# Kernel optimization log

Measured on AMD Instinct MI355X. Metric: run time of the kernel, lower is better.

## Reference

```python
import jax, jax.numpy as jnp
import numpy as np

N_NODES = 50000
N_EDGES = 800000
NFEAT = 512
NHID = 64
NHEADS = 8
NCLASS = 40
ALPHA = 0.2  # LeakyReLU slope
EPS = 1e-16  # guards isolated-node division


def setup_inputs() -> dict:
    key = jax.random.key(0)
    k = jax.random.split(key, 6)
    x = jax.random.normal(k[0], (N_NODES, NFEAT), dtype=jnp.float32)
    W_heads = jax.random.normal(k[1], (NHEADS, NFEAT, NHID), dtype=jnp.float32) * 0.05
    a_heads = jax.random.normal(k[2], (NHEADS, 2 * NHID), dtype=jnp.float32) * 0.05
    W_out = jax.random.normal(k[3], (NHEADS * NHID, NCLASS), dtype=jnp.float32) * 0.05
    a_out = jax.random.normal(k[4], (2 * NCLASS,), dtype=jnp.float32) * 0.05
    edge_index = jax.random.randint(k[5], (2, N_EDGES), 0, N_NODES, dtype=jnp.int32)
    return {"x": x, "W_heads": W_heads, "a_heads": a_heads,
            "W_out": W_out, "a_out": a_out, "edge_index": edge_index}


def _gat_layer(x, W, a, row, col, concat):
    # pyGAT sparse layer: h = xW; e_ij = exp(-LeakyReLU(a^T [h_i || h_j]));
    # out_i = sum_j e_ij h_j / sum_j e_ij   (aggregate into row, gather from col)
    D = W.shape[1]
    h = x @ W                                            # [N, D]
    score = h[row] @ a[:D] + h[col] @ a[D:]              # [E]
    e = jnp.exp(-jax.nn.leaky_relu(score, ALPHA))        # [E]
    num = jax.ops.segment_sum(e[:, None] * h[col], row, num_segments=x.shape[0])  # [N, D]
    den = jax.ops.segment_sum(e, row, num_segments=x.shape[0])                    # [N]
    out = num / (den[:, None] + EPS)
    return jax.nn.elu(out) if concat else out


def reference(x, W_heads, a_heads, W_out, a_out, edge_index):
    # dropout layers are identity in eval mode (training=False)
    row, col = edge_index[0], edge_index[1]
    heads = jax.vmap(lambda W, a: _gat_layer(x, W, a, row, col, True))(W_heads, a_heads)
    # [H, N, D] -> [N, H*D] (concat along feature dim, head-major like torch.cat)
    hcat = jnp.transpose(heads, (1, 0, 2)).reshape(x.shape[0], -1)
    return _gat_layer(hcat, W_out, a_out, row, col, False)  # [N, NCLASS]
```

## Files before the change

kernel.cpp:

```cpp
#include <hip/hip_runtime.h>
#include <hip/hip_bf16.h>

#define N_NODES 50000
#define N_EDGES 800000
#define NFEAT   512
#define NHID    64
#define NHEADS  8
#define NCLASS  40
#define HD      (NHEADS*NHID)
#define ALPHA   0.2f
#define EPS_F   1e-16f
#define NCHUNK  ((N_NODES + 255)/256)

typedef __attribute__((ext_vector_type(8))) short short8;
typedef __attribute__((ext_vector_type(4))) float floatx4;

__device__ __forceinline__ float bf2f(unsigned short u) {
    union { unsigned int i; float f; } v; v.i = ((unsigned int)u) << 16; return v.f;
}
__device__ __forceinline__ unsigned short f2bf(float f) {
    union { __hip_bfloat16 h; unsigned short u; } cv;
    cv.h = __float2bfloat16(f);
    return cv.u;
}

__global__ void prep(const float* __restrict__ Wh, unsigned short* __restrict__ Wrb,
                     const float* __restrict__ Wo, unsigned short* __restrict__ Wob,
                     int* __restrict__ deg) {
    int idx = blockIdx.x*256 + threadIdx.x;
    if (idx >= 512*512) return;
    if (idx < N_NODES) deg[idx] = 0;
    {
        int n = idx >> 9, k = idx & 511;
        int hd = n >> 6, d = n & 63;
        Wrb[idx] = f2bf(Wh[(size_t)hd*NFEAT*NHID + (size_t)k*NHID + d]);
    }
    if (idx < 64*512) {
        int n = idx >> 9, k = idx & 511;
        float v = (n < NCLASS) ? Wo[(size_t)k*NCLASS + n] : 0.f;
        Wob[idx] = f2bf(v);
    }
}

__global__ __launch_bounds__(256) void mfma_gemm1(const float* __restrict__ A,
                                                  const unsigned short* __restrict__ Bbf,
                                                  unsigned short* __restrict__ H1p, int M) {
    int id = blockIdx.x;
    int rb = (id >> 5)*8 + (id & 7);
    int cb = (id >> 3) & 3;
    int row0 = rb * 128, col0 = cb * 128;
    if (row0 >= M) return;

    __shared__ short Asl[128*40];
    __shared__ short Bsl[128*40];
    int tid  = threadIdx.x;
    int wid  = tid >> 6, lane = tid & 63;
    int lrow = lane & 15, quad = lane >> 4;
    int wm = wid & 1, wn = wid >> 1;

    int sr[2], sk[2];
#pragma unroll
    for (int it = 0; it < 2; ++it) {
        int q = tid + it*256;
        sr[it] = q >> 2; sk[it] = (q & 3) * 8;
    }
    int arow[2];
#pragma unroll
    for (int it = 0; it < 2; ++it) {
        int ar = row0 + sr[it];
        arow[it] = ar < M ? ar : M - 1;
    }

    floatx4 acc[4][4];
#pragma unroll
    for (int mm = 0; mm < 4; mm++)
#pragma unroll
        for (int nn = 0; nn < 4; nn++) acc[mm][nn] = (floatx4){0.f,0.f,0.f,0.f};

    float4 fa[2][2];
    short8 fb[2];
#pragma unroll
    for (int it = 0; it < 2; ++it) {
        const float* src = A + (size_t)arow[it]*512 + sk[it];
        fa[it][0] = *(const float4*)src;
        fa[it][1] = *(const float4*)(src + 4);
        fb[it] = *(const short8*)(Bbf + (size_t)(col0 + sr[it])*512 + sk[it]);
    }

    for (int k0 = 0; k0 < 512; k0 += 32) {
#pragma unroll
        for (int it = 0; it < 2; ++it) {
            short8 h;
            h[0] = (short)f2bf(fa[it][0].x); h[1] = (short)f2bf(fa[it][0].y);
            h[2] = (short)f2bf(fa[it][0].z); h[3] = (short)f2bf(fa[it][0].w);
            h[4] = (short)f2bf(fa[it][1].x); h[5] = (short)f2bf(fa[it][1].y);
            h[6] = (short)f2bf(fa[it][1].z); h[7] = (short)f2bf(fa[it][1].w);
            *(short8*)(&Asl[sr[it]*40 + sk[it]]) = h;
            *(short8*)(&Bsl[sr[it]*40 + sk[it]]) = fb[it];
        }
        __syncthreads();
        if (k0 + 32 < 512) {
            int kn = k0 + 32;
#pragma unroll
            for (int it = 0; it < 2; ++it) {
                const float* src = A + (size_t)arow[it]*512 + kn + sk[it];
                fa[it][0] = *(const float4*)src;
                fa[it][1] = *(const float4*)(src + 4);
                fb[it] = *(const short8*)(Bbf + (size_t)(col0 + sr[it])*512 + kn + sk[it]);
            }
        }
        short8 af[4], bfr[4];
#pragma unroll
        for (int mm = 0; mm < 4; ++mm)
            af[mm] = *(const short8*)(&Asl[(wm*64 + mm*16 + lrow)*40 + quad*8]);
#pragma unroll
        for (int nn = 0; nn < 4; ++nn)
            bfr[nn] = *(const short8*)(&Bsl[(wn*64 + nn*16 + lrow)*40 + quad*8]);
#pragma unroll
        for (int mm = 0; mm < 4; ++mm)
#pragma unroll
            for (int nn = 0; nn < 4; ++nn)
                acc[mm][nn] = __builtin_amdgcn_mfma_f32_16x16x32_bf16(
                    af[mm], bfr[nn], acc[mm][nn], 0, 0, 0);
        __syncthreads();
    }

#pragma unroll
    for (int mm = 0; mm < 4; ++mm) {
        int rbase = row0 + wm*64 + mm*16 + quad*4;
#pragma unroll
        for (int nn = 0; nn < 4; ++nn) {
            int c = col0 + wn*64 + nn*16 + lrow;
            int off = (c & 63)*8 + (c >> 6);
#pragma unroll
            for (int r = 0; r < 4; ++r) {
                int grow = rbase + r;
                if (grow < M)
                    H1p[(size_t)grow*512 + off] = f2bf(acc[mm][nn][r]);
            }
        }
    }
}

__global__ __launch_bounds__(256) void mfma_gemm2(const unsigned short* __restrict__ Abf,
                                                  const unsigned short* __restrict__ Bbf,
                                                  float* __restrict__ H2p, int M) {
    __shared__ short Asl[256*40];
    __shared__ short Bsl[64*40];
    int tid  = threadIdx.x;
    int wid  = tid >> 6, lane = tid & 63;
    int lrow = lane & 15, quad = lane >> 4;
    int row0 = blockIdx.x * 256;

    floatx4 acc[4][4];
#pragma unroll
    for (int mm = 0; mm < 4; mm++)
#pragma unroll
        for (int nn = 0; nn < 4; nn++) acc[mm][nn] = (floatx4){0.f,0.f,0.f,0.f};

    for (int k0 = 0; k0 < 512; k0 += 32) {
#pragma unroll
        for (int it = 0; it < 4; ++it) {
            int q  = tid + it*256;
            int r  = q >> 2, kk = (q & 3) * 8;
            int ar = row0 + r; ar = ar < M ? ar : M - 1;
            *(short8*)(&Asl[r*40 + kk]) =
                *(const short8*)(Abf + (size_t)ar*512 + k0 + kk);
        }
        {
            int r = tid >> 2, kk = (tid & 3) * 8;
            *(short8*)(&Bsl[r*40 + kk]) =
                *(const short8*)(Bbf + (size_t)r*512 + k0 + kk);
        }
        __syncthreads();
        short8 af[4], bfr[4];
#pragma unroll
        for (int mm = 0; mm < 4; ++mm)
            af[mm] = *(const short8*)(&Asl[(wid*64 + mm*16 + lrow)*40 + quad*8]);
#pragma unroll
        for (int nn = 0; nn < 4; ++nn)
            bfr[nn] = *(const short8*)(&Bsl[(nn*16 + lrow)*40 + quad*8]);
#pragma unroll
        for (int mm = 0; mm < 4; ++mm)
#pragma unroll
            for (int nn = 0; nn < 4; ++nn)
                acc[mm][nn] = __builtin_amdgcn_mfma_f32_16x16x32_bf16(
                    af[mm], bfr[nn], acc[mm][nn], 0, 0, 0);
        __syncthreads();
    }

#pragma unroll
    for (int mm = 0; mm < 4; ++mm) {
        int rbase = row0 + wid*64 + mm*16 + quad*4;
#pragma unroll
        for (int nn = 0; nn < 4; ++nn) {
            int c = nn*16 + lrow;
#pragma unroll
            for (int r = 0; r < 4; ++r) {
                int grow = rbase + r;
                if (grow < M)
                    H2p[(size_t)grow*64 + c] = acc[mm][nn][r];
            }
        }
    }
}

__global__ __launch_bounds__(256) void dots1(const unsigned short* __restrict__ H1p,
                                             const float* __restrict__ a_heads,
                                             float* __restrict__ srcdot,
                                             float* __restrict__ dstdot) {
    int wave = (blockIdx.x*256 + threadIdx.x) >> 6;
    int lane = threadIdx.x & 63;
    if (wave >= N_NODES) return;
    short8 hv = *(const short8*)(H1p + (size_t)wave*512 + lane*8);
    float s0[8], s1[8];
#pragma unroll
    for (int j = 0; j < 8; j++) {
        float h = bf2f((unsigned short)hv[j]);
        s0[j] = h * a_heads[j*128 + lane];
        s1[j] = h * a_heads[j*128 + 64 + lane];
    }
#pragma unroll
    for (int off = 32; off > 0; off >>= 1) {
#pragma unroll
        for (int j = 0; j < 8; j++) {
            s0[j] += __shfl_down(s0[j], off, 64);
            s1[j] += __shfl_down(s1[j], off, 64);
        }
    }
    if (lane == 0) {
#pragma unroll
        for (int j = 0; j < 8; j++) {
            srcdot[wave*8 + j] = s0[j];
            dstdot[wave*8 + j] = s1[j];
        }
    }
}

__global__ void histk(const int* __restrict__ row, int* __restrict__ deg) {
    int e = blockIdx.x*256 + threadIdx.x;
    if (e < N_EDGES) atomicAdd(&deg[row[e]], 1);
}
__global__ void scanA(const int* __restrict__ deg, int* __restrict__ row_ptr,
                      int* __restrict__ chunk_tot) {
    __shared__ int s[256];
    int t = threadIdx.x;
    int idx = blockIdx.x*256 + t;
    int v = (idx < N_NODES) ? deg[idx] : 0;
    s[t] = v;
    __syncthreads();
#pragma unroll
    for (int off = 1; off < 256; off <<= 1) {
        int x = (t >= off) ? s[t-off] : 0;
        __syncthreads();
        s[t] += x;
        __syncthreads();
    }
    if (idx < N_NODES) row_ptr[idx] = s[t] - v;
    if (t == 255) chunk_tot[blockIdx.x] = s[t];
}
__global__ void scanB(const int* __restrict__ chunk_tot, int* __restrict__ chunk_off,
                      int* __restrict__ row_ptr) {
    __shared__ int s[256];
    int t = threadIdx.x;
    int v = (t < NCHUNK) ? chunk_tot[t] : 0;
    s[t] = v;
    __syncthreads();
#pragma unroll
    for (int off = 1; off < 256; off <<= 1) {
        int x = (t >= off) ? s[t-off] : 0;
        __syncthreads();
        s[t] += x;
        __syncthreads();
    }
    if (t < NCHUNK) chunk_off[t] = s[t] - v;
    if (t == 255) row_ptr[N_NODES] = s[t];
}
__global__ void scanC(const int* __restrict__ chunk_off, int* __restrict__ row_ptr,
                      int* __restrict__ cursor) {
    int idx = blockIdx.x*256 + threadIdx.x;
    if (idx < N_NODES) {
        int rp = row_ptr[idx] + chunk_off[idx >> 8];
        row_ptr[idx] = rp;
        cursor[idx] = rp;
    }
}

__global__ void fillk_w1(const int* __restrict__ row, const int* __restrict__ col,
                         const float* __restrict__ srcdot, const float* __restrict__ dstdot,
                         int* __restrict__ cursor, int* __restrict__ csr_col,
                         float* __restrict__ Wcsr) {
    int e = blockIdx.x*256 + threadIdx.x;
    if (e >= N_EDGES) return;
    int r = row[e], c = col[e];
    int pos = atomicAdd(&cursor[r], 1);
    csr_col[pos] = c;
    float4 sa = *(const float4*)(srcdot + (size_t)r*8);
    float4 sb = *(const float4*)(srcdot + (size_t)r*8 + 4);
    float4 da = *(const float4*)(dstdot + (size_t)c*8);
    float4 db = *(const float4*)(dstdot + (size_t)c*8 + 4);
    float s[8] = {sa.x+da.x, sa.y+da.y, sa.z+da.z, sa.w+da.w,
                  sb.x+db.x, sb.y+db.y, sb.z+db.z, sb.w+db.w};
    float o[8];
#pragma unroll
    for (int j = 0; j < 8; j++) {
        float lr = s[j] > 0.f ? s[j] : ALPHA*s[j];
        o[j] = __expf(-lr);
    }
    *(float4*)(Wcsr + (size_t)pos*8)     = make_float4(o[0], o[1], o[2], o[3]);
    *(float4*)(Wcsr + (size_t)pos*8 + 4) = make_float4(o[4], o[5], o[6], o[7]);
}

__global__ __launch_bounds__(256) void agg1(const unsigned short* __restrict__ H1p,
                                            const float* __restrict__ Wcsr,
                                            const int* __restrict__ row_ptr,
                                            const int* __restrict__ csr_col,
                                            unsigned short* __restrict__ hcatb) {
    int wave = (blockIdx.x*256 + threadIdx.x) >> 6;
    int lane = threadIdx.x & 63;
    if (wave >= N_NODES) return;
    int start = row_ptr[wave], end = row_ptr[wave+1];
    float acc[8], den[8];
#pragma unroll
    for (int j = 0; j < 8; j++) { acc[j] = 0.f; den[j] = 0.f; }

    int k = start;
    for (; k + 4 <= end; k += 4) {
        int c0 = csr_col[k],   c1 = csr_col[k+1];
        int c2 = csr_col[k+2], c3 = csr_col[k+3];
        short8 hv0 = *(const short8*)(H1p + (size_t)c0*512 + lane*8);
        short8 hv1 = *(const short8*)(H1p + (size_t)c1*512 + lane*8);
        short8 hv2 = *(const short8*)(H1p + (size_t)c2*512 + lane*8);
        short8 hv3 = *(const short8*)(H1p + (size_t)c3*512 + lane*8);
        float4 wv[8];
#pragma unroll
        for (int q = 0; q < 8; q++)
            wv[q] = *(const float4*)(Wcsr + (size_t)k*8 + q*4);
        const float* w0 = (const float*)&wv[0];
        const float* w1 = (const float*)&wv[2];
        const float* w2 = (const float*)&wv[4];
        const float* w3 = (const float*)&wv[6];
#pragma unroll
        for (int j = 0; j < 8; j++) {
            den[j] += (w0[j] + w1[j]) + (w2[j] + w3[j]);
            acc[j] = fmaf(w0[j], bf2f((unsigned short)hv0[j]), acc[j]);
            acc[j] = fmaf(w1[j], bf2f((unsigned short)hv1[j]), acc[j]);
            acc[j] = fmaf(w2[j], bf2f((unsigned short)hv2[j]), acc[j]);
            acc[j] = fmaf(w3[j], bf2f((unsigned short)hv3[j]), acc[j]);
        }
    }
    for (; k < end; ++k) {
        int c = csr_col[k];
        float4 wa = *(const float4*)(Wcsr + (size_t)k*8);
        float4 wb = *(const float4*)(Wcsr + (size_t)k*8 + 4);
        short8 hv = *(const short8*)(H1p + (size_t)c*512 + lane*8);
        float w[8] = {wa.x, wa.y, wa.z, wa.w, wb.x, wb.y, wb.z, wb.w};
#pragma unroll
        for (int j = 0; j < 8; j++) {
            den[j] += w[j];
            acc[j] = fmaf(w[j], bf2f((unsigned short)hv[j]), acc[j]);
        }
    }
#pragma unroll
    for (int j = 0; j < 8; j++) {
        float o = acc[j] / (den[j] + EPS_F);
        o = o > 0.f ? o : (__expf(o) - 1.f);
        hcatb[(size_t)wave*HD + j*64 + lane] = f2bf(o);
    }
}

__global__ void dots2(const float* __restrict__ H2p, const float* __restrict__ a_out,
                      float* __restrict__ src2, float* __restrict__ dst2) {
    int i = blockIdx.x*256 + threadIdx.x;
    if (i >= N_NODES) return;
    float s0 = 0.f, s1 = 0.f;
#pragma unroll
    for (int c = 0; c < NCLASS; c++) {
        float h = H2p[(size_t)i*64 + c];
        s0 = fmaf(h, a_out[c], s0);
        s1 = fmaf(h, a_out[NCLASS + c], s1);
    }
    src2[i] = s0; dst2[i] = s1;
}

__global__ __launch_bounds__(256) void agg2(const float* __restrict__ H2p,
                                            const float* __restrict__ src2,
                                            const float* __restrict__ dst2,
                                            const int* __restrict__ row_ptr,
                                            const int* __restrict__ csr_col,
                                            float* __restrict__ out) {
    int wave = (blockIdx.x*256 + threadIdx.x) >> 6;
    int lane = threadIdx.x & 63;
    if (wave >= N_NODES) return;
    int start = row_ptr[wave], end = row_ptr[wave+1];
    float s2i = src2[wave];
    int l = lane < NCLASS ? lane : 0;
    float acc = 0.f, den = 0.f;
    int k = start;
    for (; k + 4 <= end; k += 4) {
        int c0 = csr_col[k],   c1 = csr_col[k+1];
        int c2 = csr_col[k+2], c3 = csr_col[k+3];
        float t0 = s2i + dst2[c0], t1 = s2i + dst2[c1];
        float t2 = s2i + dst2[c2], t3 = s2i + dst2[c3];
        float h0 = H2p[(size_t)c0*64 + l];
        float h1 = H2p[(size_t)c1*64 + l];
        float h2 = H2p[(size_t)c2*64 + l];
        float h3 = H2p[(size_t)c3*64 + l];
        t0 = t0 > 0.f ? t0 : ALPHA*t0;  float w0 = __expf(-t0);
        t1 = t1 > 0.f ? t1 : ALPHA*t1;  float w1 = __expf(-t1);
        t2 = t2 > 0.f ? t2 : ALPHA*t2;  float w2 = __expf(-t2);
        t3 = t3 > 0.f ? t3 : ALPHA*t3;  float w3 = __expf(-t3);
        den += (w0 + w1) + (w2 + w3);
        acc = fmaf(w0, h0, acc);
        acc = fmaf(w1, h1, acc);
        acc = fmaf(w2, h2, acc);
        acc = fmaf(w3, h3, acc);
    }
    for (; k < end; ++k) {
        int c = csr_col[k];
        float t = s2i + dst2[c];
        t = t > 0.f ? t : ALPHA*t;
        float w = __expf(-t);
        den += w;
        acc = fmaf(w, H2p[(size_t)c*64 + l], acc);
    }
    if (lane < NCLASS)
        out[(size_t)wave*NCLASS + lane] = acc / (den + EPS_F);
}

extern "C" void kernel_launch(void* const* d_in, const int* in_sizes, int n_in,
                              void* d_out, int out_size, void* d_ws, size_t ws_size,
                              hipStream_t stream) {
    const float* x       = (const float*)d_in[0];
    const float* W_heads = (const float*)d_in[1];
    const float* a_heads = (const float*)d_in[2];
    const float* W_out   = (const float*)d_in[3];
    const float* a_out   = (const float*)d_in[4];
    const int*   ei      = (const int*)d_in[5];
    const int*   row     = ei;
    const int*   col     = ei + N_EDGES;
    float* out = (float*)d_out;

    char* ws = (char*)d_ws;
    size_t off = 0;
    auto alloc = [&](size_t bytes) {
        char* p = ws + off;
        off = (off + bytes + 255) & ~(size_t)255;
        return p;
    };
    unsigned short* Wrb   = (unsigned short*)alloc((size_t)512*512*2);
    unsigned short* Wob   = (unsigned short*)alloc((size_t)64*512*2);
    unsigned short* H1p   = (unsigned short*)alloc((size_t)N_NODES*HD*2);
    unsigned short* hcatb = (unsigned short*)alloc((size_t)N_NODES*HD*2);
    float* srcdot  = (float*)alloc((size_t)N_NODES*NHEADS*4);
    float* dstdot  = (float*)alloc((size_t)N_NODES*NHEADS*4);
    float* Wcsr    = (float*)alloc((size_t)N_EDGES*NHEADS*4);
    int*   deg     = (int*)alloc((size_t)N_NODES*4);
    int*   row_ptr = (int*)alloc((size_t)(N_NODES+1)*4);
    int*   cursor  = (int*)alloc((size_t)N_NODES*4);
    int*   ctot    = (int*)alloc(256*4);
    int*   coff    = (int*)alloc(256*4);
    int*   csr_col = (int*)alloc((size_t)N_EDGES*4);
    float* H2p     = (float*)alloc((size_t)N_NODES*64*4);
    float* src2    = (float*)alloc((size_t)N_NODES*4);
    float* dst2    = (float*)alloc((size_t)N_NODES*4);
    (void)ws_size;

    const int EB = (N_EDGES + 255)/256;
    const int WB = (N_NODES*64 + 255)/256;
    const int NB = (N_NODES + 255)/256;

    prep<<<(512*512 + 255)/256, 256, 0, stream>>>(W_heads, Wrb, W_out, Wob, deg);
    {
        int rtiles = (N_NODES + 127)/128;
        int nblk = ((rtiles + 7)/8) * 32;
        mfma_gemm1<<<nblk, 256, 0, stream>>>(x, Wrb, H1p, N_NODES);
    }
    dots1<<<WB, 256, 0, stream>>>(H1p, a_heads, srcdot, dstdot);

    histk<<<EB, 256, 0, stream>>>(row, deg);
    scanA<<<NCHUNK, 256, 0, stream>>>(deg, row_ptr, ctot);
    scanB<<<1, 256, 0, stream>>>(ctot, coff, row_ptr);
    scanC<<<NCHUNK, 256, 0, stream>>>(coff, row_ptr, cursor);
    fillk_w1<<<EB, 256, 0, stream>>>(row, col, srcdot, dstdot, cursor,
                                     csr_col, Wcsr);

    agg1<<<WB, 256, 0, stream>>>(H1p, Wcsr, row_ptr, csr_col, hcatb);

    mfma_gemm2<<<(N_NODES + 255)/256, 256, 0, stream>>>(hcatb, Wob, H2p, N_NODES);
    dots2<<<NB, 256, 0, stream>>>(H2p, a_out, src2, dst2);
    agg2<<<WB, 256, 0, stream>>>(H2p, src2, dst2, row_ptr, csr_col, out);
}
```

Baseline: 551.6 us.

## Compute edge attention weights inside agg1, preload columns via readlane, pipeline gathers

Stops materializing per-edge attention weights (Wcsr) in the CSR fill kernel. agg1 now recomputes them on the fly from srcdot and gathered dstdot. Both aggregation kernels load up to 64 neighbor indices once per wave into a register, broadcast them with readlane, and double-buffer the gathers so the next batch loads while the current one is consumed. dots2 moves to one wave per node with a shuffle reduction. The aim is to cut the 25.6MB write and read of Wcsr and the serialized index loads, at the cost of redundant exp work and higher register pressure.

```diff
diff --git a/kernel.cpp b/kernel.cpp
--- a/kernel.cpp
+++ b/kernel.cpp
@@ -286,33 +286,18 @@
     }
 }
 
-__global__ void fillk_w1(const int* __restrict__ row, const int* __restrict__ col,
-                         const float* __restrict__ srcdot, const float* __restrict__ dstdot,
-                         int* __restrict__ cursor, int* __restrict__ csr_col,
-                         float* __restrict__ Wcsr) {
+__global__ void fillk(const int* __restrict__ row, const int* __restrict__ col,
+                      int* __restrict__ cursor, int* __restrict__ csr_col) {
     int e = blockIdx.x*256 + threadIdx.x;
     if (e >= N_EDGES) return;
     int r = row[e], c = col[e];
     int pos = atomicAdd(&cursor[r], 1);
     csr_col[pos] = c;
-    float4 sa = *(const float4*)(srcdot + (size_t)r*8);
-    float4 sb = *(const float4*)(srcdot + (size_t)r*8 + 4);
-    float4 da = *(const float4*)(dstdot + (size_t)c*8);
-    float4 db = *(const float4*)(dstdot + (size_t)c*8 + 4);
-    float s[8] = {sa.x+da.x, sa.y+da.y, sa.z+da.z, sa.w+da.w,
-                  sb.x+db.x, sb.y+db.y, sb.z+db.z, sb.w+db.w};
-    float o[8];
-#pragma unroll
-    for (int j = 0; j < 8; j++) {
-        float lr = s[j] > 0.f ? s[j] : ALPHA*s[j];
-        o[j] = __expf(-lr);
-    }
-    *(float4*)(Wcsr + (size_t)pos*8)     = make_float4(o[0], o[1], o[2], o[3]);
-    *(float4*)(Wcsr + (size_t)pos*8 + 4) = make_float4(o[4], o[5], o[6], o[7]);
 }
 
 __global__ __launch_bounds__(256) void agg1(const unsigned short* __restrict__ H1p,
-                                            const float* __restrict__ Wcsr,
+                                            const float* __restrict__ srcdot,
+                                            const float* __restrict__ dstdot,
                                             const int* __restrict__ row_ptr,
                                             const int* __restrict__ csr_col,
                                             unsigned short* __restrict__ hcatb) {
@@ -320,67 +305,123 @@
     int lane = threadIdx.x & 63;
     if (wave >= N_NODES) return;
     int start = row_ptr[wave], end = row_ptr[wave+1];
-    float acc[8], den[8];
-#pragma unroll
-    for (int j = 0; j < 8; j++) { acc[j] = 0.f; den[j] = 0.f; }
-
+    int deg = end - start;
+
+    float4 sa = *(const float4*)(srcdot + (size_t)wave*8);
+    float4 sb = *(const float4*)(srcdot + (size_t)wave*8 + 4);
+    float sd0 = sa.x, sd1 = sa.y, sd2 = sa.z, sd3 = sa.w;
+    float sd4 = sb.x, sd5 = sb.y, sd6 = sb.z, sd7 = sb.w;
+
+    float acc0=0.f,acc1=0.f,acc2=0.f,acc3=0.f,acc4=0.f,acc5=0.f,acc6=0.f,acc7=0.f;
+    float den0=0.f,den1=0.f,den2=0.f,den3=0.f,den4=0.f,den5=0.f,den6=0.f,den7=0.f;
+
+    int colreg = 0;
+    if (deg > 0) colreg = csr_col[start + (lane < deg ? lane : deg - 1)];
+
+#define CONS1(H, D0, D1) do { \
+    float t0_=sd0+(D0).x, t1_=sd1+(D0).y, t2_=sd2+(D0).z, t3_=sd3+(D0).w; \
+    float t4_=sd4+(D1).x, t5_=sd5+(D1).y, t6_=sd6+(D1).z, t7_=sd7+(D1).w; \
+    t0_ = t0_>0.f?t0_:ALPHA*t0_; t1_ = t1_>0.f?t1_:ALPHA*t1_; \
+    t2_ = t2_>0.f?t2_:ALPHA*t2_; t3_ = t3_>0.f?t3_:ALPHA*t3_; \
+    t4_ = t4_>0.f?t4_:ALPHA*t4_; t5_ = t5_>0.f?t5_:ALPHA*t5_; \
+    t6_ = t6_>0.f?t6_:ALPHA*t6_; t7_ = t7_>0.f?t7_:ALPHA*t7_; \
+    float w0_=__expf(-t0_), w1_=__expf(-t1_), w2_=__expf(-t2_), w3_=__expf(-t3_); \
+    float w4_=__expf(-t4_), w5_=__expf(-t5_), w6_=__expf(-t6_), w7_=__expf(-t7_); \
+    den0+=w0_; acc0=fmaf(w0_, bf2f((unsigned short)(H)[0]), acc0); \
+    den1+=w1_; acc1=fmaf(w1_, bf2f((unsigned short)(H)[1]), acc1); \
+    den2+=w2_; acc2=fmaf(w2_, bf2f((unsigned short)(H)[2]), acc2); \
+    den3+=w3_; acc3=fmaf(w3_, bf2f((unsigned short)(H)[3]), acc3); \
+    den4+=w4_; acc4=fmaf(w4_, bf2f((unsigned short)(H)[4]), acc4); \
+    den5+=w5_; acc5=fmaf(w5_, bf2f((unsigned short)(H)[5]), acc5); \
+    den6+=w6_; acc6=fmaf(w6_, bf2f((unsigned short)(H)[6]), acc6); \
+    den7+=w7_; acc7=fmaf(w7_, bf2f((unsigned short)(H)[7]), acc7); \
+} while(0)
+
+#define GATH3(HS0,HS1,HS2,P0,P1,P2,P3,P4,P5,BASE) do { \
+    int cg0_ = __builtin_amdgcn_readlane(colreg, (BASE)); \
+    int cg1_ = __builtin_amdgcn_readlane(colreg, (BASE)+1); \
+    int cg2_ = __builtin_amdgcn_readlane(colreg, (BASE)+2); \
+    HS0 = *(const short8*)(H1p + (size_t)cg0_*512 + lane*8); \
+    P0  = *(const float4*)(dstdot + (size_t)cg0_*8); \
+    P1  = *(const float4*)(dstdot + (size_t)cg0_*8 + 4); \
+    HS1 = *(const short8*)(H1p + (size_t)cg1_*512 + lane*8); \
+    P2  = *(const float4*)(dstdot + (size_t)cg1_*8); \
+    P3  = *(const float4*)(dstdot + (size_t)cg1_*8 + 4); \
+    HS2 = *(const short8*)(H1p + (size_t)cg2_*512 + lane*8); \
+    P4  = *(const float4*)(dstdot + (size_t)cg2_*8); \
+    P5  = *(const float4*)(dstdot + (size_t)cg2_*8 + 4); \
+} while(0)
+
+#define CONS3(HS0,HS1,HS2,P0,P1,P2,P3,P4,P5) do { \
+    CONS1(HS0,P0,P1); CONS1(HS1,P2,P3); CONS1(HS2,P4,P5); } while(0)
+
+    int lim = deg < 64 ? deg : 64;
+    int nb = lim / 3;
     int k = start;
-    for (; k + 4 <= end; k += 4) {
-        int c0 = csr_col[k],   c1 = csr_col[k+1];
-        int c2 = csr_col[k+2], c3 = csr_col[k+3];
-        short8 hv0 = *(const short8*)(H1p + (size_t)c0*512 + lane*8);
-        short8 hv1 = *(const short8*)(H1p + (size_t)c1*512 + lane*8);
-        short8 hv2 = *(const short8*)(H1p + (size_t)c2*512 + lane*8);
-        short8 hv3 = *(const short8*)(H1p + (size_t)c3*512 + lane*8);
-        float4 wv[8];
-#pragma unroll
-        for (int q = 0; q < 8; q++)
-            wv[q] = *(const float4*)(Wcsr + (size_t)k*8 + q*4);
-        const float* w0 = (const float*)&wv[0];
-        const float* w1 = (const float*)&wv[2];
-        const float* w2 = (const float*)&wv[4];
-        const float* w3 = (const float*)&wv[6];
+    short8 ha0, ha1, ha2, hb0, hb1, hb2;
+    float4 pa0, pa1, pa2, pa3, pa4, pa5;
+    float4 pb0, pb1, pb2, pb3, pb4, pb5;
+    if (nb > 0) {
+        GATH3(ha0,ha1,ha2, pa0,pa1,pa2,pa3,pa4,pa5, 0);
+        int b = 1;
+        for (; b + 1 < nb; b += 2) {
+            GATH3(hb0,hb1,hb2, pb0,pb1,pb2,pb3,pb4,pb5, b*3);
+            CONS3(ha0,ha1,ha2, pa0,pa1,pa2,pa3,pa4,pa5);
+            GATH3(ha0,ha1,ha2, pa0,pa1,pa2,pa3,pa4,pa5, (b+1)*3);
+            CONS3(hb0,hb1,hb2, pb0,pb1,pb2,pb3,pb4,pb5);
+        }
+        if (b < nb) {
+            GATH3(hb0,hb1,hb2, pb0,pb1,pb2,pb3,pb4,pb5, b*3);
+            CONS3(ha0,ha1,ha2, pa0,pa1,pa2,pa3,pa4,pa5);
+            CONS3(hb0,hb1,hb2, pb0,pb1,pb2,pb3,pb4,pb5);
+        } else {
+            CONS3(ha0,ha1,ha2, pa0,pa1,pa2,pa3,pa4,pa5);
+        }
+        k = start + nb*3;
+    }
+    for (; k < end; ++k) {
+        int c_ = (k - start < 64) ? __builtin_amdgcn_readlane(colreg, k - start)
+                                  : csr_col[k];
+        short8 hv = *(const short8*)(H1p + (size_t)c_*512 + lane*8);
+        float4 d0 = *(const float4*)(dstdot + (size_t)c_*8);
+        float4 d1 = *(const float4*)(dstdot + (size_t)c_*8 + 4);
+        CONS1(hv, d0, d1);
+    }
+#undef GATH3
+#undef CONS3
+
+    {
+        float o, dsum;
+        float accv[8] = {acc0,acc1,acc2,acc3,acc4,acc5,acc6,acc7};
+        float denv[8] = {den0,den1,den2,den3,den4,den5,den6,den7};
 #pragma unroll
         for (int j = 0; j < 8; j++) {
-            den[j] += (w0[j] + w1[j]) + (w2[j] + w3[j]);
-            acc[j] = fmaf(w0[j], bf2f((unsigned short)hv0[j]), acc[j]);
-            acc[j] = fmaf(w1[j], bf2f((unsigned short)hv1[j]), acc[j]);
-            acc[j] = fmaf(w2[j], bf2f((unsigned short)hv2[j]), acc[j]);
-            acc[j] = fmaf(w3[j], bf2f((unsigned short)hv3[j]), acc[j]);
-        }
-    }
-    for (; k < end; ++k) {
-        int c = csr_col[k];
-        float4 wa = *(const float4*)(Wcsr + (size_t)k*8);
-        float4 wb = *(const float4*)(Wcsr + (size_t)k*8 + 4);
-        short8 hv = *(const short8*)(H1p + (size_t)c*512 + lane*8);
-        float w[8] = {wa.x, wa.y, wa.z, wa.w, wb.x, wb.y, wb.z, wb.w};
-#pragma unroll
-        for (int j = 0; j < 8; j++) {
-            den[j] += w[j];
-            acc[j] = fmaf(w[j], bf2f((unsigned short)hv[j]), acc[j]);
-        }
-    }
-#pragma unroll
-    for (int j = 0; j < 8; j++) {
-        float o = acc[j] / (den[j] + EPS_F);
-        o = o > 0.f ? o : (__expf(o) - 1.f);
-        hcatb[(size_t)wave*HD + j*64 + lane] = f2bf(o);
-    }
-}
-
-__global__ void dots2(const float* __restrict__ H2p, const float* __restrict__ a_out,
-                      float* __restrict__ src2, float* __restrict__ dst2) {
-    int i = blockIdx.x*256 + threadIdx.x;
-    if (i >= N_NODES) return;
-    float s0 = 0.f, s1 = 0.f;
-#pragma unroll
-    for (int c = 0; c < NCLASS; c++) {
-        float h = H2p[(size_t)i*64 + c];
-        s0 = fmaf(h, a_out[c], s0);
-        s1 = fmaf(h, a_out[NCLASS + c], s1);
-    }
-    src2[i] = s0; dst2[i] = s1;
+            dsum = denv[j];
+            o = accv[j] / (dsum + EPS_F);
+            o = o > 0.f ? o : (__expf(o) - 1.f);
+            hcatb[(size_t)wave*HD + j*64 + lane] = f2bf(o);
+        }
+    }
+#undef CONS1
+}
+
+__global__ __launch_bounds__(256) void dots2(const float* __restrict__ H2p,
+                                             const float* __restrict__ a_out,
+                                             float* __restrict__ src2,
+                                             float* __restrict__ dst2) {
+    int wave = (blockIdx.x*256 + threadIdx.x) >> 6;
+    int lane = threadIdx.x & 63;
+    if (wave >= N_NODES) return;
+    float h  = H2p[(size_t)wave*64 + lane];
+    float a0 = lane < NCLASS ? a_out[lane] : 0.f;
+    float a1 = lane < NCLASS ? a_out[NCLASS + lane] : 0.f;
+    float s0 = h * a0, s1 = h * a1;
+#pragma unroll
+    for (int off = 32; off > 0; off >>= 1) {
+        s0 += __shfl_down(s0, off, 64);
+        s1 += __shfl_down(s1, off, 64);
+    }
+    if (lane == 0) { src2[wave] = s0; dst2[wave] = s1; }
 }
 
 __global__ __launch_bounds__(256) void agg2(const float* __restrict__ H2p,
@@ -393,37 +434,71 @@
     int lane = threadIdx.x & 63;
     if (wave >= N_NODES) return;
     int start = row_ptr[wave], end = row_ptr[wave+1];
+    int deg = end - start;
     float s2i = src2[wave];
     int l = lane < NCLASS ? lane : 0;
     float acc = 0.f, den = 0.f;
+
+    int colreg = 0;
+    if (deg > 0) colreg = csr_col[start + (lane < deg ? lane : deg - 1)];
+
+#define AG2_G1(T, H, IDX) do { \
+    int cg_ = __builtin_amdgcn_readlane(colreg, (IDX)); \
+    T = dst2[cg_]; \
+    H = H2p[(size_t)cg_*64 + l]; \
+} while(0)
+#define AG2_C1(T, H) do { \
+    float t_ = s2i + (T); \
+    t_ = t_ > 0.f ? t_ : ALPHA*t_; \
+    float w_ = __expf(-t_); \
+    den += w_; acc = fmaf(w_, (H), acc); \
+} while(0)
+#define AG2_G8(T0,T1,T2,T3,T4,T5,T6,T7,H0,H1,H2,H3,H4,H5,H6,H7,BASE) do { \
+    AG2_G1(T0,H0,(BASE));   AG2_G1(T1,H1,(BASE)+1); \
+    AG2_G1(T2,H2,(BASE)+2); AG2_G1(T3,H3,(BASE)+3); \
+    AG2_G1(T4,H4,(BASE)+4); AG2_G1(T5,H5,(BASE)+5); \
+    AG2_G1(T6,H6,(BASE)+6); AG2_G1(T7,H7,(BASE)+7); \
+} while(0)
+#define AG2_C8(T0,T1,T2,T3,T4,T5,T6,T7,H0,H1,H2,H3,H4,H5,H6,H7) do { \
+    AG2_C1(T0,H0); AG2_C1(T1,H1); AG2_C1(T2,H2); AG2_C1(T3,H3); \
+    AG2_C1(T4,H4); AG2_C1(T5,H5); AG2_C1(T6,H6); AG2_C1(T7,H7); \
+} while(0)
+
+    int lim = deg < 64 ? deg : 64;
+    int nb = lim >> 3;
     int k = start;
-    for (; k + 4 <= end; k += 4) {
-        int c0 = csr_col[k],   c1 = csr_col[k+1];
-        int c2 = csr_col[k+2], c3 = csr_col[k+3];
-        float t0 = s2i + dst2[c0], t1 = s2i + dst2[c1];
-        float t2 = s2i + dst2[c2], t3 = s2i + dst2[c3];
-        float h0 = H2p[(size_t)c0*64 + l];
-        float h1 = H2p[(size_t)c1*64 + l];
-        float h2 = H2p[(size_t)c2*64 + l];
-        float h3 = H2p[(size_t)c3*64 + l];
-        t0 = t0 > 0.f ? t0 : ALPHA*t0;  float w0 = __expf(-t0);
-        t1 = t1 > 0.f ? t1 : ALPHA*t1;  float w1 = __expf(-t1);
-        t2 = t2 > 0.f ? t2 : ALPHA*t2;  float w2 = __expf(-t2);
-        t3 = t3 > 0.f ? t3 : ALPHA*t3;  float w3 = __expf(-t3);
-        den += (w0 + w1) + (w2 + w3);
-        acc = fmaf(w0, h0, acc);
-        acc = fmaf(w1, h1, acc);
-        acc = fmaf(w2, h2, acc);
-        acc = fmaf(w3, h3, acc);
+    float ta0,ta1,ta2,ta3,ta4,ta5,ta6,ta7, ga0,ga1,ga2,ga3,ga4,ga5,ga6,ga7;
+    float tb0,tb1,tb2,tb3,tb4,tb5,tb6,tb7, gb0,gb1,gb2,gb3,gb4,gb5,gb6,gb7;
+    if (nb > 0) {
+        AG2_G8(ta0,ta1,ta2,ta3,ta4,ta5,ta6,ta7, ga0,ga1,ga2,ga3,ga4,ga5,ga6,ga7, 0);
+        int b = 1;
+        for (; b + 1 < nb; b += 2) {
+            AG2_G8(tb0,tb1,tb2,tb3,tb4,tb5,tb6,tb7, gb0,gb1,gb2,gb3,gb4,gb5,gb6,gb7, b*8);
+            AG2_C8(ta0,ta1,ta2,ta3,ta4,ta5,ta6,ta7, ga0,ga1,ga2,ga3,ga4,ga5,ga6,ga7);
+            AG2_G8(ta0,ta1,ta2,ta3,ta4,ta5,ta6,ta7, ga0,ga1,ga2,ga3,ga4,ga5,ga6,ga7, (b+1)*8);
+            AG2_C8(tb0,tb1,tb2,tb3,tb4,tb5,tb6,tb7, gb0,gb1,gb2,gb3,gb4,gb5,gb6,gb7);
+        }
+        if (b < nb) {
+            AG2_G8(tb0,tb1,tb2,tb3,tb4,tb5,tb6,tb7, gb0,gb1,gb2,gb3,gb4,gb5,gb6,gb7, b*8);
+            AG2_C8(ta0,ta1,ta2,ta3,ta4,ta5,ta6,ta7, ga0,ga1,ga2,ga3,ga4,ga5,ga6,ga7);
+            AG2_C8(tb0,tb1,tb2,tb3,tb4,tb5,tb6,tb7, gb0,gb1,gb2,gb3,gb4,gb5,gb6,gb7);
+        } else {
+            AG2_C8(ta0,ta1,ta2,ta3,ta4,ta5,ta6,ta7, ga0,ga1,ga2,ga3,ga4,ga5,ga6,ga7);
+        }
+        k = start + nb*8;
     }
     for (; k < end; ++k) {
-        int c = csr_col[k];
-        float t = s2i + dst2[c];
-        t = t > 0.f ? t : ALPHA*t;
-        float w = __expf(-t);
-        den += w;
-        acc = fmaf(w, H2p[(size_t)c*64 + l], acc);
-    }
+        int c_ = (k - start < 64) ? __builtin_amdgcn_readlane(colreg, k - start)
+                                  : csr_col[k];
+        float t = dst2[c_];
+        float h = H2p[(size_t)c_*64 + l];
+        AG2_C1(t, h);
+    }
+#undef AG2_G1
+#undef AG2_C1
+#undef AG2_G8
+#undef AG2_C8
+
     if (lane < NCLASS)
         out[(size_t)wave*NCLASS + lane] = acc / (den + EPS_F);
 }
@@ -454,7 +529,6 @@
     unsigned short* hcatb = (unsigned short*)alloc((size_t)N_NODES*HD*2);
     float* srcdot  = (float*)alloc((size_t)N_NODES*NHEADS*4);
     float* dstdot  = (float*)alloc((size_t)N_NODES*NHEADS*4);
-    float* Wcsr    = (float*)alloc((size_t)N_EDGES*NHEADS*4);
     int*   deg     = (int*)alloc((size_t)N_NODES*4);
     int*   row_ptr = (int*)alloc((size_t)(N_NODES+1)*4);
     int*   cursor  = (int*)alloc((size_t)N_NODES*4);
@@ -468,7 +542,6 @@
 
     const int EB = (N_EDGES + 255)/256;
     const int WB = (N_NODES*64 + 255)/256;
-    const int NB = (N_NODES + 255)/256;
 
     prep<<<(512*512 + 255)/256, 256, 0, stream>>>(W_heads, Wrb, W_out, Wob, deg);
     {
@@ -482,12 +555,11 @@
     scanA<<<NCHUNK, 256, 0, stream>>>(deg, row_ptr, ctot);
     scanB<<<1, 256, 0, stream>>>(ctot, coff, row_ptr);
     scanC<<<NCHUNK, 256, 0, stream>>>(coff, row_ptr, cursor);
-    fillk_w1<<<EB, 256, 0, stream>>>(row, col, srcdot, dstdot, cursor,
-                                     csr_col, Wcsr);
-
-    agg1<<<WB, 256, 0, stream>>>(H1p, Wcsr, row_ptr, csr_col, hcatb);
+    fillk<<<EB, 256, 0, stream>>>(row, col, cursor, csr_col);
+
+    agg1<<<WB, 256, 0, stream>>>(H1p, srcdot, dstdot, row_ptr, csr_col, hcatb);
 
     mfma_gemm2<<<(N_NODES + 255)/256, 256, 0, stream>>>(hcatb, Wob, H2p, N_NODES);
-    dots2<<<NB, 256, 0, stream>>>(H2p, a_out, src2, dst2);
+    dots2<<<WB, 256, 0, stream>>>(H2p, a_out, src2, dst2);
     agg2<<<WB, 256, 0, stream>>>(H2p, src2, dst2, row_ptr, csr_col, out);
 }
```

New measurement: 565.8 us. 2.6% more time.

## Fuse attention dot products into GEMM epilogues and pipeline agg2 gathers

Applied to the files above, without the earlier changes.

Computes the per-head source and destination attention dot products directly from the MFMA accumulators in both GEMM epilogues, using 16-lane xor shuffles, and removes the separate dots1 and dots2 kernels. This avoids re-reading H1p and H2p and saves two launches. agg2 now loads up to 64 column indices into a register once, broadcasts them with readlane, and software-pipelines gathers in batches of 8 with double buffering to raise memory-level parallelism. The cost is higher register pressure, and the dot products now use fp32 accumulators instead of bf16-rounded values, which slightly changes numerics.

```diff
diff --git a/kernel.cpp b/kernel.cpp
--- a/kernel.cpp
+++ b/kernel.cpp
@@ -44,7 +44,10 @@
 
 __global__ __launch_bounds__(256) void mfma_gemm1(const float* __restrict__ A,
                                                   const unsigned short* __restrict__ Bbf,
-                                                  unsigned short* __restrict__ H1p, int M) {
+                                                  const float* __restrict__ a_heads,
+                                                  unsigned short* __restrict__ H1p,
+                                                  float* __restrict__ srcdot,
+                                                  float* __restrict__ dstdot, int M) {
     int id = blockIdx.x;
     int rb = (id >> 5)*8 + (id & 7);
     int cb = (id >> 3) & 3;
@@ -125,6 +128,39 @@
         __syncthreads();
     }
 
+    {
+        int head = (col0 >> 6) + wn;
+        float a0v[4], a1v[4];
+#pragma unroll
+        for (int nn = 0; nn < 4; ++nn) {
+            a0v[nn] = a_heads[head*128 + nn*16 + lrow];
+            a1v[nn] = a_heads[head*128 + 64 + nn*16 + lrow];
+        }
+#pragma unroll
+        for (int mm = 0; mm < 4; ++mm) {
+#pragma unroll
+            for (int r = 0; r < 4; ++r) {
+                float s0 = 0.f, s1 = 0.f;
+#pragma unroll
+                for (int nn = 0; nn < 4; ++nn) {
+                    float v = acc[mm][nn][r];
+                    s0 = fmaf(v, a0v[nn], s0);
+                    s1 = fmaf(v, a1v[nn], s1);
+                }
+#pragma unroll
+                for (int off = 1; off < 16; off <<= 1) {
+                    s0 += __shfl_xor(s0, off, 64);
+                    s1 += __shfl_xor(s1, off, 64);
+                }
+                int grow = row0 + wm*64 + mm*16 + quad*4 + r;
+                if (lrow == 0 && grow < M) {
+                    srcdot[(size_t)grow*8 + head] = s0;
+                    dstdot[(size_t)grow*8 + head] = s1;
+                }
+            }
+        }
+    }
+
 #pragma unroll
     for (int mm = 0; mm < 4; ++mm) {
         int rbase = row0 + wm*64 + mm*16 + quad*4;
@@ -144,7 +180,10 @@
 
 __global__ __launch_bounds__(256) void mfma_gemm2(const unsigned short* __restrict__ Abf,
                                                   const unsigned short* __restrict__ Bbf,
-                                                  float* __restrict__ H2p, int M) {
+                                                  const float* __restrict__ a_out,
+                                                  float* __restrict__ H2p,
+                                                  float* __restrict__ src2,
+                                                  float* __restrict__ dst2, int M) {
     __shared__ short Asl[256*40];
     __shared__ short Bsl[64*40];
     int tid  = threadIdx.x;
@@ -189,6 +228,39 @@
         __syncthreads();
     }
 
+    {
+        float a0v[4], a1v[4];
+#pragma unroll
+        for (int nn = 0; nn < 4; ++nn) {
+            int c = nn*16 + lrow;
+            a0v[nn] = c < NCLASS ? a_out[c] : 0.f;
+            a1v[nn] = c < NCLASS ? a_out[NCLASS + c] : 0.f;
+        }
+#pragma unroll
+        for (int mm = 0; mm < 4; ++mm) {
+#pragma unroll
+            for (int r = 0; r < 4; ++r) {
+                float s0 = 0.f, s1 = 0.f;
+#pragma unroll
+                for (int nn = 0; nn < 4; ++nn) {
+                    float v = acc[mm][nn][r];
+                    s0 = fmaf(v, a0v[nn], s0);
+                    s1 = fmaf(v, a1v[nn], s1);
+                }
+#pragma unroll
+                for (int off = 1; off < 16; off <<= 1) {
+                    s0 += __shfl_xor(s0, off, 64);
+                    s1 += __shfl_xor(s1, off, 64);
+                }
+                int grow = row0 + wid*64 + mm*16 + quad*4 + r;
+                if (lrow == 0 && grow < M) {
+                    src2[grow] = s0;
+                    dst2[grow] = s1;
+                }
+            }
+        }
+    }
+
 #pragma unroll
     for (int mm = 0; mm < 4; ++mm) {
         int rbase = row0 + wid*64 + mm*16 + quad*4;
@@ -201,38 +273,6 @@
                 if (grow < M)
                     H2p[(size_t)grow*64 + c] = acc[mm][nn][r];
             }
-        }
-    }
-}
-
-__global__ __launch_bounds__(256) void dots1(const unsigned short* __restrict__ H1p,
-                                             const float* __restrict__ a_heads,
-                                             float* __restrict__ srcdot,
-                                             float* __restrict__ dstdot) {
-    int wave = (blockIdx.x*256 + threadIdx.x) >> 6;
-    int lane = threadIdx.x & 63;
-    if (wave >= N_NODES) return;
-    short8 hv = *(const short8*)(H1p + (size_t)wave*512 + lane*8);
-    float s0[8], s1[8];
-#pragma unroll
-    for (int j = 0; j < 8; j++) {
-        float h = bf2f((unsigned short)hv[j]);
-        s0[j] = h * a_heads[j*128 + lane];
-        s1[j] = h * a_heads[j*128 + 64 + lane];
-    }
-#pragma unroll
-    for (int off = 32; off > 0; off >>= 1) {
-#pragma unroll
-        for (int j = 0; j < 8; j++) {
-            s0[j] += __shfl_down(s0[j], off, 64);
-            s1[j] += __shfl_down(s1[j], off, 64);
-        }
-    }
-    if (lane == 0) {
-#pragma unroll
-        for (int j = 0; j < 8; j++) {
-            srcdot[wave*8 + j] = s0[j];
-            dstdot[wave*8 + j] = s1[j];
         }
     }
 }
@@ -369,20 +409,6 @@
     }
 }
 
-__global__ void dots2(const float* __restrict__ H2p, const float* __restrict__ a_out,
-                      float* __restrict__ src2, float* __restrict__ dst2) {
-    int i = blockIdx.x*256 + threadIdx.x;
-    if (i >= N_NODES) return;
-    float s0 = 0.f, s1 = 0.f;
-#pragma unroll
-    for (int c = 0; c < NCLASS; c++) {
-        float h = H2p[(size_t)i*64 + c];
-        s0 = fmaf(h, a_out[c], s0);
-        s1 = fmaf(h, a_out[NCLASS + c], s1);
-    }
-    src2[i] = s0; dst2[i] = s1;
-}
-
 __global__ __launch_bounds__(256) void agg2(const float* __restrict__ H2p,
                                             const float* __restrict__ src2,
                                             const float* __restrict__ dst2,
@@ -393,37 +419,71 @@
     int lane = threadIdx.x & 63;
     if (wave >= N_NODES) return;
     int start = row_ptr[wave], end = row_ptr[wave+1];
+    int deg = end - start;
     float s2i = src2[wave];
     int l = lane < NCLASS ? lane : 0;
     float acc = 0.f, den = 0.f;
+
+    int colreg = 0;
+    if (deg > 0) colreg = csr_col[start + (lane < deg ? lane : deg - 1)];
+
+#define AG2_G1(T, H, IDX) do { \
+    int cg_ = __builtin_amdgcn_readlane(colreg, (IDX)); \
+    T = dst2[cg_]; \
+    H = H2p[(size_t)cg_*64 + l]; \
+} while(0)
+#define AG2_C1(T, H) do { \
+    float t_ = s2i + (T); \
+    t_ = t_ > 0.f ? t_ : ALPHA*t_; \
+    float w_ = __expf(-t_); \
+    den += w_; acc = fmaf(w_, (H), acc); \
+} while(0)
+#define AG2_G8(T0,T1,T2,T3,T4,T5,T6,T7,H0,H1,H2,H3,H4,H5,H6,H7,BASE) do { \
+    AG2_G1(T0,H0,(BASE));   AG2_G1(T1,H1,(BASE)+1); \
+    AG2_G1(T2,H2,(BASE)+2); AG2_G1(T3,H3,(BASE)+3); \
+    AG2_G1(T4,H4,(BASE)+4); AG2_G1(T5,H5,(BASE)+5); \
+    AG2_G1(T6,H6,(BASE)+6); AG2_G1(T7,H7,(BASE)+7); \
+} while(0)
+#define AG2_C8(T0,T1,T2,T3,T4,T5,T6,T7,H0,H1,H2,H3,H4,H5,H6,H7) do { \
+    AG2_C1(T0,H0); AG2_C1(T1,H1); AG2_C1(T2,H2); AG2_C1(T3,H3); \
+    AG2_C1(T4,H4); AG2_C1(T5,H5); AG2_C1(T6,H6); AG2_C1(T7,H7); \
+} while(0)
+
+    int lim = deg < 64 ? deg : 64;
+    int nb = lim >> 3;
     int k = start;
-    for (; k + 4 <= end; k += 4) {
-        int c0 = csr_col[k],   c1 = csr_col[k+1];
-        int c2 = csr_col[k+2], c3 = csr_col[k+3];
-        float t0 = s2i + dst2[c0], t1 = s2i + dst2[c1];
-        float t2 = s2i + dst2[c2], t3 = s2i + dst2[c3];
-        float h0 = H2p[(size_t)c0*64 + l];
-        float h1 = H2p[(size_t)c1*64 + l];
-        float h2 = H2p[(size_t)c2*64 + l];
-        float h3 = H2p[(size_t)c3*64 + l];
-        t0 = t0 > 0.f ? t0 : ALPHA*t0;  float w0 = __expf(-t0);
-        t1 = t1 > 0.f ? t1 : ALPHA*t1;  float w1 = __expf(-t1);
-        t2 = t2 > 0.f ? t2 : ALPHA*t2;  float w2 = __expf(-t2);
-        t3 = t3 > 0.f ? t3 : ALPHA*t3;  float w3 = __expf(-t3);
-        den += (w0 + w1) + (w2 + w3);
-        acc = fmaf(w0, h0, acc);
-        acc = fmaf(w1, h1, acc);
-        acc = fmaf(w2, h2, acc);
-        acc = fmaf(w3, h3, acc);
+    float ta0,ta1,ta2,ta3,ta4,ta5,ta6,ta7, ga0,ga1,ga2,ga3,ga4,ga5,ga6,ga7;
+    float tb0,tb1,tb2,tb3,tb4,tb5,tb6,tb7, gb0,gb1,gb2,gb3,gb4,gb5,gb6,gb7;
+    if (nb > 0) {
+        AG2_G8(ta0,ta1,ta2,ta3,ta4,ta5,ta6,ta7, ga0,ga1,ga2,ga3,ga4,ga5,ga6,ga7, 0);
+        int b = 1;
+        for (; b + 1 < nb; b += 2) {
+            AG2_G8(tb0,tb1,tb2,tb3,tb4,tb5,tb6,tb7, gb0,gb1,gb2,gb3,gb4,gb5,gb6,gb7, b*8);
+            AG2_C8(ta0,ta1,ta2,ta3,ta4,ta5,ta6,ta7, ga0,ga1,ga2,ga3,ga4,ga5,ga6,ga7);
+            AG2_G8(ta0,ta1,ta2,ta3,ta4,ta5,ta6,ta7, ga0,ga1,ga2,ga3,ga4,ga5,ga6,ga7, (b+1)*8);
+            AG2_C8(tb0,tb1,tb2,tb3,tb4,tb5,tb6,tb7, gb0,gb1,gb2,gb3,gb4,gb5,gb6,gb7);
+        }
+        if (b < nb) {
+            AG2_G8(tb0,tb1,tb2,tb3,tb4,tb5,tb6,tb7, gb0,gb1,gb2,gb3,gb4,gb5,gb6,gb7, b*8);
+            AG2_C8(ta0,ta1,ta2,ta3,ta4,ta5,ta6,ta7, ga0,ga1,ga2,ga3,ga4,ga5,ga6,ga7);
+            AG2_C8(tb0,tb1,tb2,tb3,tb4,tb5,tb6,tb7, gb0,gb1,gb2,gb3,gb4,gb5,gb6,gb7);
+        } else {
+            AG2_C8(ta0,ta1,ta2,ta3,ta4,ta5,ta6,ta7, ga0,ga1,ga2,ga3,ga4,ga5,ga6,ga7);
+        }
+        k = start + nb*8;
     }
     for (; k < end; ++k) {
-        int c = csr_col[k];
-        float t = s2i + dst2[c];
-        t = t > 0.f ? t : ALPHA*t;
-        float w = __expf(-t);
-        den += w;
-        acc = fmaf(w, H2p[(size_t)c*64 + l], acc);
-    }
+        int c_ = (k - start < 64) ? __builtin_amdgcn_readlane(colreg, k - start)
+                                  : csr_col[k];
+        float t = dst2[c_];
+        float h = H2p[(size_t)c_*64 + l];
+        AG2_C1(t, h);
+    }
+#undef AG2_G1
+#undef AG2_C1
+#undef AG2_G8
+#undef AG2_C8
+
     if (lane < NCLASS)
         out[(size_t)wave*NCLASS + lane] = acc / (den + EPS_F);
 }
@@ -468,15 +528,14 @@
 
     const int EB = (N_EDGES + 255)/256;
     const int WB = (N_NODES*64 + 255)/256;
-    const int NB = (N_NODES + 255)/256;
 
     prep<<<(512*512 + 255)/256, 256, 0, stream>>>(W_heads, Wrb, W_out, Wob, deg);
     {
         int rtiles = (N_NODES + 127)/128;
         int nblk = ((rtiles + 7)/8) * 32;
-        mfma_gemm1<<<nblk, 256, 0, stream>>>(x, Wrb, H1p, N_NODES);
-    }
-    dots1<<<WB, 256, 0, stream>>>(H1p, a_heads, srcdot, dstdot);
+        mfma_gemm1<<<nblk, 256, 0, stream>>>(x, Wrb, a_heads, H1p,
+                                             srcdot, dstdot, N_NODES);
+    }
 
     histk<<<EB, 256, 0, stream>>>(row, deg);
     scanA<<<NCHUNK, 256, 0, stream>>>(deg, row_ptr, ctot);
@@ -487,7 +546,7 @@
 
     agg1<<<WB, 256, 0, stream>>>(H1p, Wcsr, row_ptr, csr_col, hcatb);
 
-    mfma_gemm2<<<(N_NODES + 255)/256, 256, 0, stream>>>(hcatb, Wob, H2p, N_NODES);
-    dots2<<<NB, 256, 0, stream>>>(H2p, a_out, src2, dst2);
+    mfma_gemm2<<<(N_NODES + 255)/256, 256, 0, stream>>>(hcatb, Wob, a_out,
+                                                        H2p, src2, dst2, N_NODES);
     agg2<<<WB, 256, 0, stream>>>(H2p, src2, dst2, row_ptr, csr_col, out);
 }
```

After: 510.1 us. 7.5% less time.
